# Kernel optimization log

Hardware: AMD Instinct MI355X
Metric: run time of the kernel (lower is better)

## Reference

```python
import jax, jax.numpy as jnp
import numpy as np
from jax import lax

NBINS = 256


def setup_inputs() -> dict:
    key = jax.random.key(0)
    y_pred = jax.random.uniform(key, (64, 3, 512, 512), dtype=jnp.float32)
    return {"y_pred": y_pred}


def reference(y_pred):
    # Faithful to: per-batch torch.histc(bins=256) (range = data min/max),
    # normalize to probs, entropy in bits with 0*log2(0)=0, mean over batch.
    B = y_pred.shape[0]
    x = y_pred.reshape(B, -1)  # [B, N]
    mn = jnp.min(x, axis=1, keepdims=True)
    mx = jnp.max(x, axis=1, keepdims=True)
    # torch.histc: if min == max they are adjusted to min-1 / max+1
    rng = jnp.where(mx > mn, mx - mn, 2.0)
    lo = jnp.where(mx > mn, mn, mn - 1.0)
    idx = jnp.clip(((x - lo) * (NBINS / rng)).astype(jnp.int32), 0, NBINS - 1)
    idx = lax.stop_gradient(idx)  # binning is non-differentiable (as in torch.histc)
    hist = jax.vmap(lambda i: jnp.bincount(i, length=NBINS))(idx)  # [B, 256]
    hist = hist.astype(y_pred.dtype)
    p = hist / jnp.sum(hist, axis=1, keepdims=True)
    safe_p = jnp.where(p == 0, 1.0, p)  # log2(1)=0 -> contributes 0
    ent = -jnp.sum(p * jnp.log2(safe_p), axis=1)  # [B], entropy in bits
    return jnp.mean(ent)
```

## Files before the change

### kernel.cpp

```cpp
#include <hip/hip_runtime.h>

#define NBINS   256
#define B       64
#define NPB     786432
#define NF4     (NPB / 4)
#define BPB     32
#define THREADS 256
#define GRID    (B * BPB)


__global__ __launch_bounds__(THREADS) void k_minmax(const float4* __restrict__ x,
                                                    float2* __restrict__ pb,
                                                    unsigned* __restrict__ hist) {
    if (blockIdx.x < B) hist[blockIdx.x * NBINS + threadIdx.x] = 0u;

    const int batch = blockIdx.x / BPB;
    const int blk   = blockIdx.x % BPB;
    const float4* p = x + (size_t)batch * NF4;

    float mn = 3.402823466e38f, mx = -3.402823466e38f;
    int t = blk * THREADS + threadIdx.x;
    #pragma unroll 4
    for (int i = t; i < NF4; i += BPB * THREADS) {
        float4 v = p[i];
        mn = fminf(mn, fminf(fminf(v.x, v.y), fminf(v.z, v.w)));
        mx = fmaxf(mx, fmaxf(fmaxf(v.x, v.y), fmaxf(v.z, v.w)));
    }
    for (int o = 32; o > 0; o >>= 1) {
        mn = fminf(mn, __shfl_down(mn, o));
        mx = fmaxf(mx, __shfl_down(mx, o));
    }
    __shared__ float smn[4], smx[4];
    int wid = threadIdx.x >> 6;
    if ((threadIdx.x & 63) == 0) { smn[wid] = mn; smx[wid] = mx; }
    __syncthreads();
    if (threadIdx.x == 0) {
        mn = fminf(fminf(smn[0], smn[1]), fminf(smn[2], smn[3]));
        mx = fmaxf(fmaxf(smx[0], smx[1]), fmaxf(smx[2], smx[3]));
        pb[blockIdx.x] = make_float2(mn, mx);
    }
}

__global__ __launch_bounds__(THREADS) void k_hist(const float4* __restrict__ x,
                                                  const float2* __restrict__ pb,
                                                  unsigned* __restrict__ hist) {
    const int batch = blockIdx.x / BPB;
    const int blk   = blockIdx.x % BPB;

    float mn = 3.402823466e38f, mx = -3.402823466e38f;
    #pragma unroll
    for (int j = 0; j < BPB; ++j) {
        float2 v = pb[batch * BPB + j];
        mn = fminf(mn, v.x);
        mx = fmaxf(mx, v.y);
    }
    const float rng   = (mx > mn) ? (mx - mn) : 2.0f;
    const float lo    = (mx > mn) ? mn : (mn - 1.0f);
    const float scale = (float)NBINS / rng;

    __shared__ unsigned lh[4][NBINS];
    for (int i = threadIdx.x; i < 4 * NBINS; i += THREADS)
        ((unsigned*)lh)[i] = 0u;
    __syncthreads();

    unsigned* h = lh[threadIdx.x >> 6];
    const float4* p = x + (size_t)batch * NF4;
    int t = blk * THREADS + threadIdx.x;
    for (int i = t; i < NF4; i += BPB * THREADS) {
        float4 v = p[i];
        int i0 = (int)((v.x - lo) * scale);
        int i1 = (int)((v.y - lo) * scale);
        int i2 = (int)((v.z - lo) * scale);
        int i3 = (int)((v.w - lo) * scale);
        i0 = min(max(i0, 0), NBINS - 1);
        i1 = min(max(i1, 0), NBINS - 1);
        i2 = min(max(i2, 0), NBINS - 1);
        i3 = min(max(i3, 0), NBINS - 1);
        atomicAdd(&h[i0], 1u);
        atomicAdd(&h[i1], 1u);
        atomicAdd(&h[i2], 1u);
        atomicAdd(&h[i3], 1u);
    }
    __syncthreads();

    unsigned* gh = hist + batch * NBINS;
    for (int i = threadIdx.x; i < NBINS; i += THREADS) {
        unsigned s = lh[0][i] + lh[1][i] + lh[2][i] + lh[3][i];
        if (s) atomicAdd(&gh[i], s);
    }
}

__global__ __launch_bounds__(THREADS) void k_entropy(const unsigned* __restrict__ hist,
                                                     float* __restrict__ out) {
    const float invN = 1.0f / (float)NPB;
    float sum = 0.0f;
    #pragma unroll 8
    for (int b = 0; b < B; ++b) {
        unsigned c = hist[b * NBINS + threadIdx.x];
        if (c) {
            float pv = (float)c * invN;
            sum += pv * log2f(pv);
        }
    }
    for (int o = 32; o > 0; o >>= 1) sum += __shfl_down(sum, o);
    __shared__ float s[4];
    int wid = threadIdx.x >> 6;
    if ((threadIdx.x & 63) == 0) s[wid] = sum;
    __syncthreads();
    if (threadIdx.x == 0)
        out[0] = -(s[0] + s[1] + s[2] + s[3]) / (float)B;
}

extern "C" void kernel_launch(void* const* d_in, const int* in_sizes, int n_in,
                              void* d_out, int out_size, void* d_ws, size_t ws_size,
                              hipStream_t stream) {
    const float4* x = (const float4*)d_in[0];
    float* out      = (float*)d_out;
    float2* pb      = (float2*)d_ws;
    unsigned* hist  = (unsigned*)((char*)d_ws + GRID * sizeof(float2));

    hipLaunchKernelGGL(k_minmax, dim3(GRID), dim3(THREADS), 0, stream,
                       x, pb, hist);
    hipLaunchKernelGGL(k_hist, dim3(GRID), dim3(THREADS), 0, stream,
                       x, pb, hist);
    hipLaunchKernelGGL(k_entropy, dim3(1), dim3(THREADS), 0, stream,
                       hist, out);
}
```

Baseline: 307.2 us.

## Fuse minmax, histogram and entropy into one kernel with per-batch spin barrier

Merges the three kernels into one persistent-style kernel. Blocks of a batch sync through an atomic counter spin-wait after the min/max pass, and the last block to finish computes the entropy. This removes the launch gaps and may let the second read of each batch's slice hit L2/MALL, since it follows the first read closely. The design relies on all 2048 blocks (8 per CU) being co-resident, otherwise the spin-wait can deadlock, and it adds a memset launch.

```diff
diff --git a/kernel.cpp b/kernel.cpp
--- a/kernel.cpp
+++ b/kernel.cpp
@@ -8,54 +8,72 @@
 #define THREADS 256
 #define GRID    (B * BPB)
 
+#define SCOPE_AGENT __HIP_MEMORY_SCOPE_AGENT
 
-__global__ __launch_bounds__(THREADS) void k_minmax(const float4* __restrict__ x,
-                                                    float2* __restrict__ pb,
-                                                    unsigned* __restrict__ hist) {
-    if (blockIdx.x < B) hist[blockIdx.x * NBINS + threadIdx.x] = 0u;
 
+__global__ __launch_bounds__(THREADS, 8) void k_fused(const float4* __restrict__ x,
+                                                      unsigned* __restrict__ ctrl,
+                                                      float* __restrict__ pb,
+                                                      unsigned* __restrict__ hist,
+                                                      float* __restrict__ out) {
     const int batch = blockIdx.x / BPB;
     const int blk   = blockIdx.x % BPB;
     const float4* p = x + (size_t)batch * NF4;
 
-    float mn = 3.402823466e38f, mx = -3.402823466e38f;
-    int t = blk * THREADS + threadIdx.x;
-    #pragma unroll 4
-    for (int i = t; i < NF4; i += BPB * THREADS) {
-        float4 v = p[i];
-        mn = fminf(mn, fminf(fminf(v.x, v.y), fminf(v.z, v.w)));
-        mx = fmaxf(mx, fmaxf(fmaxf(v.x, v.y), fmaxf(v.z, v.w)));
-    }
-    for (int o = 32; o > 0; o >>= 1) {
-        mn = fminf(mn, __shfl_down(mn, o));
-        mx = fmaxf(mx, __shfl_down(mx, o));
-    }
-    __shared__ float smn[4], smx[4];
-    int wid = threadIdx.x >> 6;
-    if ((threadIdx.x & 63) == 0) { smn[wid] = mn; smx[wid] = mx; }
-    __syncthreads();
-    if (threadIdx.x == 0) {
-        mn = fminf(fminf(smn[0], smn[1]), fminf(smn[2], smn[3]));
-        mx = fmaxf(fmaxf(smx[0], smx[1]), fmaxf(smx[2], smx[3]));
-        pb[blockIdx.x] = make_float2(mn, mx);
-    }
-}
-
-__global__ __launch_bounds__(THREADS) void k_hist(const float4* __restrict__ x,
-                                                  const float2* __restrict__ pb,
-                                                  unsigned* __restrict__ hist) {
-    const int batch = blockIdx.x / BPB;
-    const int blk   = blockIdx.x % BPB;
+    if (blk == 0)
+        __hip_atomic_store(&hist[batch * NBINS + threadIdx.x], 0u,
+                           __ATOMIC_RELAXED, SCOPE_AGENT);
 
     float mn = 3.402823466e38f, mx = -3.402823466e38f;
+    {
+        int t = blk * THREADS + threadIdx.x;
+        #pragma unroll 4
+        for (int i = t; i < NF4; i += BPB * THREADS) {
+            float4 v = p[i];
+            mn = fminf(mn, fminf(fminf(v.x, v.y), fminf(v.z, v.w)));
+            mx = fmaxf(mx, fmaxf(fmaxf(v.x, v.y), fmaxf(v.z, v.w)));
+        }
+        for (int o = 32; o > 0; o >>= 1) {
+            mn = fminf(mn, __shfl_down(mn, o));
+            mx = fmaxf(mx, __shfl_down(mx, o));
+        }
+        __shared__ float smn[4], smx[4];
+        int wid = threadIdx.x >> 6;
+        if ((threadIdx.x & 63) == 0) { smn[wid] = mn; smx[wid] = mx; }
+        __syncthreads();
+        if (threadIdx.x == 0) {
+            mn = fminf(fminf(smn[0], smn[1]), fminf(smn[2], smn[3]));
+            mx = fmaxf(fmaxf(smx[0], smx[1]), fmaxf(smx[2], smx[3]));
+            __hip_atomic_store(&pb[2 * blockIdx.x],     mn, __ATOMIC_RELAXED, SCOPE_AGENT);
+            __hip_atomic_store(&pb[2 * blockIdx.x + 1], mx, __ATOMIC_RELAXED, SCOPE_AGENT);
+        }
+    }
+
+    if (threadIdx.x == 0) {
+        __threadfence();
+        atomicAdd(&ctrl[32 + batch], 1u);
+        while (__hip_atomic_load(&ctrl[32 + batch], __ATOMIC_RELAXED, SCOPE_AGENT) < BPB)
+            __builtin_amdgcn_s_sleep(2);
+        __threadfence();
+    }
+    __syncthreads();
+
+    __shared__ float rmn[BPB], rmx[BPB];
+    if (threadIdx.x < BPB) {
+        rmn[threadIdx.x] = __hip_atomic_load(&pb[2 * (batch * BPB + threadIdx.x)],
+                                             __ATOMIC_RELAXED, SCOPE_AGENT);
+        rmx[threadIdx.x] = __hip_atomic_load(&pb[2 * (batch * BPB + threadIdx.x) + 1],
+                                             __ATOMIC_RELAXED, SCOPE_AGENT);
+    }
+    __syncthreads();
+    float bmn = rmn[0], bmx = rmx[0];
     #pragma unroll
-    for (int j = 0; j < BPB; ++j) {
-        float2 v = pb[batch * BPB + j];
-        mn = fminf(mn, v.x);
-        mx = fmaxf(mx, v.y);
+    for (int j = 1; j < BPB; ++j) {
+        bmn = fminf(bmn, rmn[j]);
+        bmx = fmaxf(bmx, rmx[j]);
     }
-    const float rng   = (mx > mn) ? (mx - mn) : 2.0f;
-    const float lo    = (mx > mn) ? mn : (mn - 1.0f);
+    const float rng   = (bmx > bmn) ? (bmx - bmn) : 2.0f;
+    const float lo    = (bmx > bmn) ? bmn : (bmn - 1.0f);
     const float scale = (float)NBINS / rng;
 
     __shared__ unsigned lh[4][NBINS];
@@ -64,22 +82,23 @@
     __syncthreads();
 
     unsigned* h = lh[threadIdx.x >> 6];
-    const float4* p = x + (size_t)batch * NF4;
-    int t = blk * THREADS + threadIdx.x;
-    for (int i = t; i < NF4; i += BPB * THREADS) {
-        float4 v = p[i];
-        int i0 = (int)((v.x - lo) * scale);
-        int i1 = (int)((v.y - lo) * scale);
-        int i2 = (int)((v.z - lo) * scale);
-        int i3 = (int)((v.w - lo) * scale);
-        i0 = min(max(i0, 0), NBINS - 1);
-        i1 = min(max(i1, 0), NBINS - 1);
-        i2 = min(max(i2, 0), NBINS - 1);
-        i3 = min(max(i3, 0), NBINS - 1);
-        atomicAdd(&h[i0], 1u);
-        atomicAdd(&h[i1], 1u);
-        atomicAdd(&h[i2], 1u);
-        atomicAdd(&h[i3], 1u);
+    {
+        int t = blk * THREADS + threadIdx.x;
+        for (int i = t; i < NF4; i += BPB * THREADS) {
+            float4 v = p[i];
+            int i0 = (int)((v.x - lo) * scale);
+            int i1 = (int)((v.y - lo) * scale);
+            int i2 = (int)((v.z - lo) * scale);
+            int i3 = (int)((v.w - lo) * scale);
+            i0 = min(max(i0, 0), NBINS - 1);
+            i1 = min(max(i1, 0), NBINS - 1);
+            i2 = min(max(i2, 0), NBINS - 1);
+            i3 = min(max(i3, 0), NBINS - 1);
+            atomicAdd(&h[i0], 1u);
+            atomicAdd(&h[i1], 1u);
+            atomicAdd(&h[i2], 1u);
+            atomicAdd(&h[i3], 1u);
+        }
     }
     __syncthreads();
 
@@ -88,27 +107,36 @@
         unsigned s = lh[0][i] + lh[1][i] + lh[2][i] + lh[3][i];
         if (s) atomicAdd(&gh[i], s);
     }
-}
+    __syncthreads();
 
-__global__ __launch_bounds__(THREADS) void k_entropy(const unsigned* __restrict__ hist,
-                                                     float* __restrict__ out) {
+    __shared__ int is_last;
+    if (threadIdx.x == 0) {
+        __threadfence();
+        unsigned t = atomicAdd(&ctrl[0], 1u);
+        is_last = (t == GRID - 1);
+        if (t == GRID - 1) __threadfence();
+    }
+    __syncthreads();
+    if (!is_last) return;
+
     const float invN = 1.0f / (float)NPB;
     float sum = 0.0f;
     #pragma unroll 8
     for (int b = 0; b < B; ++b) {
-        unsigned c = hist[b * NBINS + threadIdx.x];
+        unsigned c = __hip_atomic_load(&hist[b * NBINS + threadIdx.x],
+                                       __ATOMIC_RELAXED, SCOPE_AGENT);
         if (c) {
             float pv = (float)c * invN;
             sum += pv * log2f(pv);
         }
     }
     for (int o = 32; o > 0; o >>= 1) sum += __shfl_down(sum, o);
-    __shared__ float s[4];
+    __shared__ float s4[4];
     int wid = threadIdx.x >> 6;
-    if ((threadIdx.x & 63) == 0) s[wid] = sum;
+    if ((threadIdx.x & 63) == 0) s4[wid] = sum;
     __syncthreads();
     if (threadIdx.x == 0)
-        out[0] = -(s[0] + s[1] + s[2] + s[3]) / (float)B;
+        out[0] = -(s4[0] + s4[1] + s4[2] + s4[3]) / (float)B;
 }
 
 extern "C" void kernel_launch(void* const* d_in, const int* in_sizes, int n_in,
@@ -116,13 +144,11 @@
                               hipStream_t stream) {
     const float4* x = (const float4*)d_in[0];
     float* out      = (float*)d_out;
-    float2* pb      = (float2*)d_ws;
-    unsigned* hist  = (unsigned*)((char*)d_ws + GRID * sizeof(float2));
+    unsigned* ctrl  = (unsigned*)d_ws;
+    float* pb       = (float*)((char*)d_ws + 4096);
+    unsigned* hist  = (unsigned*)((char*)d_ws + 4096 + 2 * GRID * sizeof(float));
 
-    hipLaunchKernelGGL(k_minmax, dim3(GRID), dim3(THREADS), 0, stream,
-                       x, pb, hist);
-    hipLaunchKernelGGL(k_hist, dim3(GRID), dim3(THREADS), 0, stream,
-                       x, pb, hist);
-    hipLaunchKernelGGL(k_entropy, dim3(1), dim3(THREADS), 0, stream,
-                       hist, out);
+    hipMemsetAsync(ctrl, 0, 4096, stream);
+    hipLaunchKernelGGL(k_fused, dim3(GRID), dim3(THREADS), 0, stream,
+                       x, ctrl, pb, hist, out);
 }
```

New measurement: 620.8 us. 2.02x slower.

## Fuse entropy into histogram kernel via last-block ticket, retune grids

Applied to the files above, without the earlier changes.

Folds the single-block entropy kernel into the histogram kernel: each block takes an agent-scope atomic ticket and the last finishing block computes the entropy, removing one kernel launch. The histogram grid is halved to 16 blocks per batch with an unrolled loop, and the min/max loop is fully unrolled with two independent accumulators to expose more loads in flight. The cost is a global atomic counter and fences, plus fewer blocks and so less parallelism in the histogram pass.

```diff
diff --git a/kernel.cpp b/kernel.cpp
--- a/kernel.cpp
+++ b/kernel.cpp
@@ -4,28 +4,44 @@
 #define B       64
 #define NPB     786432
 #define NF4     (NPB / 4)
-#define BPB     32
 #define THREADS 256
-#define GRID    (B * BPB)
+
+#define BPB_MM   32
+#define GRID_MM  (B * BPB_MM)
+#define STRIDE_MM (BPB_MM * THREADS)
+
+#define BPB_H    16
+#define GRID_H   (B * BPB_H)
+#define STRIDE_H (BPB_H * THREADS)
+
+#define SCOPE_AGENT __HIP_MEMORY_SCOPE_AGENT
 
 
 __global__ __launch_bounds__(THREADS) void k_minmax(const float4* __restrict__ x,
                                                     float2* __restrict__ pb,
-                                                    unsigned* __restrict__ hist) {
+                                                    unsigned* __restrict__ hist,
+                                                    unsigned* __restrict__ ctrl) {
     if (blockIdx.x < B) hist[blockIdx.x * NBINS + threadIdx.x] = 0u;
+    if (blockIdx.x == 0 && threadIdx.x == 0) ctrl[0] = 0u;
 
-    const int batch = blockIdx.x / BPB;
-    const int blk   = blockIdx.x % BPB;
+    const int batch = blockIdx.x / BPB_MM;
+    const int blk   = blockIdx.x % BPB_MM;
     const float4* p = x + (size_t)batch * NF4;
 
-    float mn = 3.402823466e38f, mx = -3.402823466e38f;
-    int t = blk * THREADS + threadIdx.x;
-    #pragma unroll 4
-    for (int i = t; i < NF4; i += BPB * THREADS) {
-        float4 v = p[i];
-        mn = fminf(mn, fminf(fminf(v.x, v.y), fminf(v.z, v.w)));
-        mx = fmaxf(mx, fmaxf(fmaxf(v.x, v.y), fmaxf(v.z, v.w)));
+    float mnA = 3.402823466e38f, mxA = -3.402823466e38f;
+    float mnB = 3.402823466e38f, mxB = -3.402823466e38f;
+    const int t = blk * THREADS + threadIdx.x;
+    #pragma unroll
+    for (int j = 0; j < NF4 / STRIDE_MM; j += 2) {
+        float4 a = p[t + j * STRIDE_MM];
+        float4 b = p[t + (j + 1) * STRIDE_MM];
+        mnA = fminf(mnA, fminf(fminf(a.x, a.y), fminf(a.z, a.w)));
+        mxA = fmaxf(mxA, fmaxf(fmaxf(a.x, a.y), fmaxf(a.z, a.w)));
+        mnB = fminf(mnB, fminf(fminf(b.x, b.y), fminf(b.z, b.w)));
+        mxB = fmaxf(mxB, fmaxf(fmaxf(b.x, b.y), fmaxf(b.z, b.w)));
     }
+    float mn = fminf(mnA, mnB), mx = fmaxf(mxA, mxB);
+
     for (int o = 32; o > 0; o >>= 1) {
         mn = fminf(mn, __shfl_down(mn, o));
         mx = fmaxf(mx, __shfl_down(mx, o));
@@ -43,14 +59,16 @@
 
 __global__ __launch_bounds__(THREADS) void k_hist(const float4* __restrict__ x,
                                                   const float2* __restrict__ pb,
-                                                  unsigned* __restrict__ hist) {
-    const int batch = blockIdx.x / BPB;
-    const int blk   = blockIdx.x % BPB;
+                                                  unsigned* __restrict__ hist,
+                                                  unsigned* __restrict__ ctrl,
+                                                  float* __restrict__ out) {
+    const int batch = blockIdx.x / BPB_H;
+    const int blk   = blockIdx.x % BPB_H;
 
     float mn = 3.402823466e38f, mx = -3.402823466e38f;
     #pragma unroll
-    for (int j = 0; j < BPB; ++j) {
-        float2 v = pb[batch * BPB + j];
+    for (int j = 0; j < BPB_MM; ++j) {
+        float2 v = pb[batch * BPB_MM + j];
         mn = fminf(mn, v.x);
         mx = fmaxf(mx, v.y);
     }
@@ -65,8 +83,9 @@
 
     unsigned* h = lh[threadIdx.x >> 6];
     const float4* p = x + (size_t)batch * NF4;
-    int t = blk * THREADS + threadIdx.x;
-    for (int i = t; i < NF4; i += BPB * THREADS) {
+    const int t = blk * THREADS + threadIdx.x;
+    #pragma unroll 4
+    for (int i = t; i < NF4; i += STRIDE_H) {
         float4 v = p[i];
         int i0 = (int)((v.x - lo) * scale);
         int i1 = (int)((v.y - lo) * scale);
@@ -88,27 +107,36 @@
         unsigned s = lh[0][i] + lh[1][i] + lh[2][i] + lh[3][i];
         if (s) atomicAdd(&gh[i], s);
     }
-}
+    __syncthreads();
 
-__global__ __launch_bounds__(THREADS) void k_entropy(const unsigned* __restrict__ hist,
-                                                     float* __restrict__ out) {
+    __shared__ unsigned last;
+    if (threadIdx.x == 0) {
+        unsigned tk = __hip_atomic_fetch_add(&ctrl[0], 1u,
+                                             __ATOMIC_ACQ_REL, SCOPE_AGENT);
+        last = (tk == GRID_H - 1) ? 1u : 0u;
+    }
+    __syncthreads();
+    if (!last) return;
+
+    __threadfence();
     const float invN = 1.0f / (float)NPB;
     float sum = 0.0f;
     #pragma unroll 8
     for (int b = 0; b < B; ++b) {
-        unsigned c = hist[b * NBINS + threadIdx.x];
+        unsigned c = __hip_atomic_load(&hist[b * NBINS + threadIdx.x],
+                                       __ATOMIC_RELAXED, SCOPE_AGENT);
         if (c) {
             float pv = (float)c * invN;
             sum += pv * log2f(pv);
         }
     }
     for (int o = 32; o > 0; o >>= 1) sum += __shfl_down(sum, o);
-    __shared__ float s[4];
+    __shared__ float s4[4];
     int wid = threadIdx.x >> 6;
-    if ((threadIdx.x & 63) == 0) s[wid] = sum;
+    if ((threadIdx.x & 63) == 0) s4[wid] = sum;
     __syncthreads();
     if (threadIdx.x == 0)
-        out[0] = -(s[0] + s[1] + s[2] + s[3]) / (float)B;
+        out[0] = -(s4[0] + s4[1] + s4[2] + s4[3]) / (float)B;
 }
 
 extern "C" void kernel_launch(void* const* d_in, const int* in_sizes, int n_in,
@@ -116,13 +144,12 @@
                               hipStream_t stream) {
     const float4* x = (const float4*)d_in[0];
     float* out      = (float*)d_out;
-    float2* pb      = (float2*)d_ws;
-    unsigned* hist  = (unsigned*)((char*)d_ws + GRID * sizeof(float2));
+    unsigned* ctrl  = (unsigned*)d_ws;
+    float2* pb      = (float2*)((char*)d_ws + 256);
+    unsigned* hist  = (unsigned*)((char*)d_ws + 256 + GRID_MM * sizeof(float2));
 
-    hipLaunchKernelGGL(k_minmax, dim3(GRID), dim3(THREADS), 0, stream,
-                       x, pb, hist);
-    hipLaunchKernelGGL(k_hist, dim3(GRID), dim3(THREADS), 0, stream,
-                       x, pb, hist);
-    hipLaunchKernelGGL(k_entropy, dim3(1), dim3(THREADS), 0, stream,
-                       hist, out);
+    hipLaunchKernelGGL(k_minmax, dim3(GRID_MM), dim3(THREADS), 0, stream,
+                       x, pb, hist, ctrl);
+    hipLaunchKernelGGL(k_hist, dim3(GRID_H), dim3(THREADS), 0, stream,
+                       x, pb, hist, ctrl, out);
 }
```

Result: slower. 331.4 us (+7.9%).
